# Performance work log

Hardware: AMD Instinct MI355X
Metric: run time of the kernel (lower is better)

The kernel has to match this reference:

```python
import jax, jax.numpy as jnp
import numpy as np

G, NPG, C, H, F, L = 256, 128, 16, 128, 128, 3
N = G * NPG          # 32768 nodes
E = 524288           # 16 edges per node on average
REG, REG_C = 0.01, 0.01
LN_EPS = 1e-5


def setup_inputs() -> dict:
    key = jax.random.key(0)
    ks = jax.random.split(key, 20)
    x = jax.random.normal(ks[0], (N, F), dtype=jnp.float32)
    # edges kept within each graph so dense pooling matches to_dense_batch semantics
    epg = E // G
    offs = jnp.repeat(jnp.arange(G, dtype=jnp.int64) * NPG, epg)
    src = jax.random.randint(ks[1], (E,), 0, NPG, dtype=jnp.int64) + offs
    tgt = jax.random.randint(ks[2], (E,), 0, NPG, dtype=jnp.int64) + offs
    edge_index = jnp.stack([src, tgt])
    mask_breaks = jax.random.bernoulli(ks[3], 0.5, (E,))
    s = jax.random.uniform(ks[4], (N, C), dtype=jnp.float32)
    batch = jnp.repeat(jnp.arange(G, dtype=jnp.int64), NPG)
    sc = 1.0 / np.sqrt(H)
    Wn = jax.random.normal(ks[5], (L, H, H), dtype=jnp.float32) * sc
    bn_ = jax.random.normal(ks[6], (L, H), dtype=jnp.float32) * sc
    Wo = jax.random.normal(ks[7], (L, H, H), dtype=jnp.float32) * sc
    bo = jax.random.normal(ks[8], (L, H), dtype=jnp.float32) * sc
    Wr = jax.random.normal(ks[9], (L, H, H), dtype=jnp.float32) * sc
    ln_g = jnp.ones((L, H), dtype=jnp.float32)
    ln_b = jnp.zeros((L, H), dtype=jnp.float32)
    fln_g = jnp.ones((H,), dtype=jnp.float32)
    fln_b = jnp.zeros((H,), dtype=jnp.float32)
    lin_w = jax.random.normal(ks[10], (1, H), dtype=jnp.float32) * sc
    bias = jnp.zeros((1,), dtype=jnp.float32)
    return {"x": x, "edge_index": edge_index, "mask_breaks": mask_breaks, "s": s,
            "batch": batch, "Wn": Wn, "bn_": bn_, "Wo": Wo, "bo": bo, "Wr": Wr,
            "ln_g": ln_g, "ln_b": ln_b, "fln_g": fln_g, "fln_b": fln_b,
            "lin_w": lin_w, "bias": bias}


def _layernorm(h, g, b):
    mu = jnp.mean(h, axis=-1, keepdims=True)
    v = jnp.mean(jnp.square(h - mu), axis=-1, keepdims=True)
    return (h - mu) * jax.lax.rsqrt(v + LN_EPS) * g + b


def reference(x, edge_index, mask_breaks, s, batch, Wn, bn_, Wo, bo, Wr,
              ln_g, ln_b, fln_g, fln_b, lin_w, bias):
    src, tgt = edge_index[0], edge_index[1]
    ones_e = jnp.ones((E,), dtype=x.dtype)
    cnt = jax.ops.segment_sum(ones_e, tgt, num_segments=N)          # in-degree
    inv_cnt = (1.0 / jnp.maximum(cnt, 1.0))[:, None]
    h = x
    for i in range(L):
        x_in = h @ Wn[i].T + bn_[i]
        x_out = h @ Wo[i].T + bo[i]
        x_root = h @ Wr[i].T
        msg = jnp.where(mask_breaks[:, None], x_in[src], x_out[src])  # [E,H]
        agg = jax.ops.segment_sum(msg, tgt, num_segments=N) * inv_cnt  # mean aggr
        h = jax.nn.relu(_layernorm(agg + x_root, ln_g[i], ln_b[i]))
    # dense per-graph views (equal-size graphs, batch ids sorted -> reshape)
    xd = h.reshape(G, NPG, H)
    sd = s.reshape(G, NPG, C)
    pooled = jnp.einsum("gnc,gnh->gch", sd, xd)                      # [G,C,H]
    pooled = _layernorm(pooled, fln_g, fln_b)
    xc = pooled @ lin_w.T                                            # [G,C,1]
    col_sum = sd.sum(axis=1)                                          # [G,C]
    cmask = (col_sum > 0)[..., None]
    xc = xc * cmask.astype(xc.dtype)
    out = xc.sum(axis=1) + bias                                      # [G,1]
    reg_loss = jnp.abs(Wo).sum() + jnp.abs(bo).sum()
    denom = (cmask.astype(xc.dtype).squeeze(-1) + 1e-7).sum(axis=1, keepdims=True)
    l1_loss = (jnp.abs(xc).sum(axis=1) / denom).mean()
    losses = REG * reg_loss + REG_C * l1_loss
    return out, losses, xc
```

## Files before the change

kernel.cpp:

```cpp
#include <hip/hip_runtime.h>

#define NN   32768
#define HD   128
#define EE   524288
#define GG   256
#define EPG  2048
#define CCd  16
#define LLd  3

typedef short short8 __attribute__((ext_vector_type(8)));
typedef float f32x4 __attribute__((ext_vector_type(4)));

__device__ __forceinline__ unsigned short f2bf(float f) {
  unsigned u = __builtin_bit_cast(unsigned, f);
  return (unsigned short)((u + 0x7FFFu + ((u >> 16) & 1u)) >> 16);
}
__device__ __forceinline__ unsigned bfpack(float a, float b) {
  return (unsigned)f2bf(a) | ((unsigned)f2bf(b) << 16);
}

__global__ __launch_bounds__(256) void convert_w_kernel(const float* __restrict__ Wn, const float* __restrict__ Wo,
                                                        const float* __restrict__ Wr, const float* __restrict__ bo,
                                                        unsigned* __restrict__ Wnb, unsigned* __restrict__ Wob,
                                                        unsigned* __restrict__ Wrb, float* __restrict__ wsreg) {
  int i = blockIdx.x * 256 + threadIdx.x;
  float4 a = *(const float4*)(Wn + (size_t)i * 4);
  float4 b = *(const float4*)(Wo + (size_t)i * 4);
  float4 c = *(const float4*)(Wr + (size_t)i * 4);
  *(uint2*)(Wnb + (size_t)i * 2) = make_uint2(bfpack(a.x, a.y), bfpack(a.z, a.w));
  *(uint2*)(Wob + (size_t)i * 2) = make_uint2(bfpack(b.x, b.y), bfpack(b.z, b.w));
  *(uint2*)(Wrb + (size_t)i * 2) = make_uint2(bfpack(c.x, c.y), bfpack(c.z, c.w));
  float s = fabsf(b.x) + fabsf(b.y) + fabsf(b.z) + fabsf(b.w);
  if (blockIdx.x == 0 && threadIdx.x < 96) {
    float4 d = *(const float4*)(bo + threadIdx.x * 4);
    s += fabsf(d.x) + fabsf(d.y) + fabsf(d.z) + fabsf(d.w);
  }
#pragma unroll
  for (int mk = 1; mk < 64; mk <<= 1) s += __shfl_xor(s, mk, 64);
  if ((threadIdx.x & 63) == 0) atomicAdd(wsreg, s);
}

__global__ __launch_bounds__(512, 2) void fused_kernel(
    const float* __restrict__ x,
    const int* __restrict__ esrc, const int* __restrict__ etgt, const int* __restrict__ emask,
    const unsigned short* __restrict__ Wnb, const unsigned short* __restrict__ Wob,
    const unsigned short* __restrict__ Wrb,
    const float* __restrict__ bn, const float* __restrict__ bo,
    const float* __restrict__ lng, const float* __restrict__ lnb,
    const float* __restrict__ s,
    const float* __restrict__ flng, const float* __restrict__ flnb,
    const float* __restrict__ linw, const float* __restrict__ bias,
    float* __restrict__ out, float* __restrict__ l1g) {
  __shared__ __align__(16) unsigned short hTs[128 * 136];
  __shared__ __align__(16) unsigned short sTs[16 * 136];
  __shared__ __align__(16) unsigned Mlds[2 * 128 * 64];
  __shared__ __align__(16) unsigned Wlds[128 * 64];
  __shared__ float finS[128], foutS[128];
  __shared__ float colsumS[CCd], xcs[CCd], axcs[CCd], msk[CCd];

  const int g = blockIdx.x;
  const int tid = threadIdx.x;
  const int wave = tid >> 6;
  const int lane = tid & 63;
  const int m = lane & 15;
  const int q = lane >> 4;
  const int t0 = wave << 4;

  const int wr = tid >> 2, wq = tid & 3, wsw = wr & 7;
  const int wbase = wr * 16 + wq * 4;
  uint4 wv0, wv1, wv2, wv3;
  {
    const uint4* wp = (const uint4*)Wnb;
    wv0 = wp[wbase + 0]; wv1 = wp[wbase + 1]; wv2 = wp[wbase + 2]; wv3 = wp[wbase + 3];
  }
  auto w_store = [&]() {
    *(uint4*)&Wlds[wr * 64 + (((wq * 4 + 0) ^ wsw) << 2)] = wv0;
    *(uint4*)&Wlds[wr * 64 + (((wq * 4 + 1) ^ wsw) << 2)] = wv1;
    *(uint4*)&Wlds[wr * 64 + (((wq * 4 + 2) ^ wsw) << 2)] = wv2;
    *(uint4*)&Wlds[wr * 64 + (((wq * 4 + 3) ^ wsw) << 2)] = wv3;
  };
  auto w_load = [&](const unsigned short* Wg) {
    const uint4* wp = (const uint4*)Wg;
    wv0 = wp[wbase + 0]; wv1 = wp[wbase + 1]; wv2 = wp[wbase + 2]; wv3 = wp[wbase + 3];
  };

  {
    uint4* cz = (uint4*)Mlds;
#pragma unroll
    for (int i = 0; i < 8; ++i) cz[i * 512 + tid] = make_uint4(0u, 0u, 0u, 0u);

    const float4* xg = (const float4*)(x + (size_t)g * 16384);
#pragma unroll
    for (int i = 0; i < 8; ++i) {
      int flat = i * 512 + tid;
      int t = flat >> 5, f0 = (flat & 31) << 2;
      float4 v = xg[flat];
      hTs[(f0 + 0) * 136 + t] = f2bf(v.x);
      hTs[(f0 + 1) * 136 + t] = f2bf(v.y);
      hTs[(f0 + 2) * 136 + t] = f2bf(v.z);
      hTs[(f0 + 3) * 136 + t] = f2bf(v.w);
    }
    {
      int t = tid >> 2, c0 = (tid & 3) << 2;
      float4 v = *(const float4*)(s + (size_t)g * 2048 + t * 16 + c0);
      sTs[(c0 + 0) * 136 + t] = f2bf(v.x);
      sTs[(c0 + 1) * 136 + t] = f2bf(v.y);
      sTs[(c0 + 2) * 136 + t] = f2bf(v.z);
      sTs[(c0 + 3) * 136 + t] = f2bf(v.w);
    }
    if (tid < 64) {
      int c = tid & 15, qq = tid >> 4;
      float cs = 0.f;
      for (int tt = qq; tt < 128; tt += 4) cs += s[(size_t)g * 2048 + tt * 16 + c];
      cs += __shfl_xor(cs, 16); cs += __shfl_xor(cs, 32);
      if (qq == 0) colsumS[c] = cs;
    }
  }
  __syncthreads();

  {
    const int e0 = g * EPG;
#pragma unroll
    for (int i = 0; i < 4; ++i) {
      int e = e0 + i * 512 + tid;
      int t = etgt[e] & 127;
      int sl = esrc[e] & 127;
      int dir = (emask[e] != 0) ? 0 : 1;
      atomicAdd(&Mlds[dir * 8192 + t * 64 + (((sl >> 3) ^ (t & 7)) << 2) + ((sl >> 1) & 3)],
                1u << ((sl & 1) * 16));
    }
  }
  __syncthreads();

  {
    const int t = t0 + m;
    const int base0 = t * 64 + q * 16;
    unsigned nin = 0, nout = 0;
#pragma unroll
    for (int k4 = 0; k4 < 4; ++k4) {
      uint4 a = *(const uint4*)&Mlds[base0 + k4 * 4];
      uint4 b = *(const uint4*)&Mlds[8192 + base0 + k4 * 4];
      nin  += (a.x & 0xffffu) + (a.x >> 16) + (a.y & 0xffffu) + (a.y >> 16)
            + (a.z & 0xffffu) + (a.z >> 16) + (a.w & 0xffffu) + (a.w >> 16);
      nout += (b.x & 0xffffu) + (b.x >> 16) + (b.y & 0xffffu) + (b.y >> 16)
            + (b.z & 0xffffu) + (b.z >> 16) + (b.w & 0xffffu) + (b.w >> 16);
    }
    nin  += __shfl_xor((int)nin, 16);  nin  += __shfl_xor((int)nin, 32);
    nout += __shfl_xor((int)nout, 16); nout += __shfl_xor((int)nout, 32);
    unsigned dg = nin + nout;
    float inv = 1.0f / (float)(dg > 0 ? dg : 1);
    if (q == 0) { finS[t] = (float)nin * inv; foutS[t] = (float)nout * inv; }
#pragma unroll
    for (int d = 0; d < 2; ++d)
#pragma unroll
      for (int k4 = 0; k4 < 4; ++k4) {
        unsigned* p = &Mlds[d * 8192 + base0 + k4 * 4];
        uint4 v = *(const uint4*)p;
        uint4 o;
        o.x = bfpack((float)(v.x & 0xffffu) * inv, (float)(v.x >> 16) * inv);
        o.y = bfpack((float)(v.y & 0xffffu) * inv, (float)(v.y >> 16) * inv);
        o.z = bfpack((float)(v.z & 0xffffu) * inv, (float)(v.z >> 16) * inv);
        o.w = bfpack((float)(v.w & 0xffffu) * inv, (float)(v.w >> 16) * inv);
        *(uint4*)p = o;
      }
  }
  __syncthreads();

  for (int L = 0; L < LLd; ++L) {
    f32x4 pre[8];
#pragma unroll
    for (int ct = 0; ct < 8; ++ct) pre[ct] = (f32x4){0.f, 0.f, 0.f, 0.f};
    f32x4 accT[8];

#pragma unroll
    for (int sg = 0; sg < 2; ++sg) {
#pragma unroll
      for (int ft = 0; ft < 8; ++ft) accT[ft] = (f32x4){0.f, 0.f, 0.f, 0.f};
#pragma unroll
      for (int hf = 0; hf < 2; ++hf)
#pragma unroll
        for (int ksl = 0; ksl < 2; ++ksl) {
          const int ksg = hf * 2 + ksl;
          short8 bfr = *(const short8*)&Mlds[sg * 8192 + (t0 + m) * 64 + (((ksg * 4 + q) ^ (m & 7)) << 2)];
#pragma unroll
          for (int ft = 0; ft < 8; ++ft) {
            short8 afr = *(const short8*)&hTs[(ft * 16 + m) * 136 + ksg * 32 + q * 8];
            accT[ft] = __builtin_amdgcn_mfma_f32_16x16x32_bf16(afr, bfr, accT[ft], 0, 0, 0);
          }
        }
      __syncthreads();
      w_store();
      w_load((sg == 0 ? Wob : Wrb) + L * 16384);
      __syncthreads();
#pragma unroll
      for (int hf = 0; hf < 2; ++hf)
#pragma unroll
        for (int ksl = 0; ksl < 2; ++ksl) {
          const int ksg = hf * 2 + ksl;
          f32x4 lo = accT[2 * ksg], hi = accT[2 * ksg + 1];
          short8 afr;
#pragma unroll
          for (int j = 0; j < 8; ++j) {
            int srcl = ((((q & 1) << 1) + (j >> 2)) << 4) + m;
            float ylo = __shfl(lo[j & 3], srcl, 64);
            float yhi = __shfl(hi[j & 3], srcl, 64);
            afr[j] = (short)f2bf((q >> 1) ? yhi : ylo);
          }
#pragma unroll
          for (int ct = 0; ct < 8; ++ct) {
            short8 bfr = *(const short8*)&Wlds[(ct * 16 + m) * 64 + (((ksg * 4 + q) ^ (m & 7)) << 2)];
            pre[ct] = __builtin_amdgcn_mfma_f32_16x16x32_bf16(afr, bfr, pre[ct], 0, 0, 0);
          }
        }
    }
    __syncthreads();
    w_store();
    if (L < LLd - 1) w_load(Wnb + (L + 1) * 16384);
    __syncthreads();
#pragma unroll
    for (int hf = 0; hf < 2; ++hf)
#pragma unroll
      for (int ksl = 0; ksl < 2; ++ksl) {
        const int ksg = hf * 2 + ksl;
        short8 afr;
#pragma unroll
        for (int j = 0; j < 8; ++j)
          afr[j] = (short)hTs[(ksg * 32 + q * 8 + j) * 136 + t0 + m];
#pragma unroll
        for (int ct = 0; ct < 8; ++ct) {
          short8 bfr = *(const short8*)&Wlds[(ct * 16 + m) * 64 + (((ksg * 4 + q) ^ (m & 7)) << 2)];
          pre[ct] = __builtin_amdgcn_mfma_f32_16x16x32_bf16(afr, bfr, pre[ct], 0, 0, 0);
        }
      }
    __syncthreads();
    {
      float bnv[8], bov[8], gv[8], bv[8];
#pragma unroll
      for (int ct = 0; ct < 8; ++ct) {
        int c = L * 128 + ct * 16 + m;
        bnv[ct] = bn[c]; bov[ct] = bo[c]; gv[ct] = lng[c]; bv[ct] = lnb[c];
      }
#pragma unroll
      for (int r = 0; r < 4; ++r) {
        const int tl = q * 4 + r;
        const float fiv = finS[t0 + tl], fov = foutS[t0 + tl];
        float v[8];
        float sum = 0.f;
#pragma unroll
        for (int ct = 0; ct < 8; ++ct) {
          v[ct] = pre[ct][r] + fiv * bnv[ct] + fov * bov[ct];
          sum += v[ct];
        }
        sum += __shfl_xor(sum, 1); sum += __shfl_xor(sum, 2);
        sum += __shfl_xor(sum, 4); sum += __shfl_xor(sum, 8);
        const float mu = sum * (1.0f / 128.0f);
        float sq = 0.f;
#pragma unroll
        for (int ct = 0; ct < 8; ++ct) { float d = v[ct] - mu; sq += d * d; }
        sq += __shfl_xor(sq, 1); sq += __shfl_xor(sq, 2);
        sq += __shfl_xor(sq, 4); sq += __shfl_xor(sq, 8);
        const float rstd = rsqrtf(sq * (1.0f / 128.0f) + 1e-5f);
#pragma unroll
        for (int ct = 0; ct < 8; ++ct) {
          float o = fmaxf((v[ct] - mu) * rstd * gv[ct] + bv[ct], 0.0f);
          hTs[(ct * 16 + m) * 136 + t0 + tl] = f2bf(o);
        }
      }
    }
    __syncthreads();
  }

  f32x4 pl = (f32x4){0.f, 0.f, 0.f, 0.f};
#pragma unroll
  for (int ks = 0; ks < 4; ++ks) {
    short8 a = *(const short8*)&sTs[m * 136 + ks * 32 + q * 8];
    short8 b = *(const short8*)&hTs[(wave * 16 + m) * 136 + ks * 32 + q * 8];
    pl = __builtin_amdgcn_mfma_f32_16x16x32_bf16(a, b, pl, 0, 0, 0);
  }
  float* pooledS = (float*)Mlds;
#pragma unroll
  for (int r = 0; r < 4; ++r) pooledS[(q * 4 + r) * 132 + wave * 16 + m] = pl[r];
  __syncthreads();

  if (tid < 256) {
    const int c = tid >> 4;
    const int j0 = (tid & 15) << 3;
    float v[8];
#pragma unroll
    for (int jj = 0; jj < 8; ++jj) v[jj] = pooledS[c * 132 + j0 + jj];
    float sum = 0.f;
#pragma unroll
    for (int jj = 0; jj < 8; ++jj) sum += v[jj];
#pragma unroll
    for (int mk = 1; mk < 16; mk <<= 1) sum += __shfl_xor(sum, mk, 64);
    float mu = sum * (1.0f / 128.0f);
    float sq = 0.f;
#pragma unroll
    for (int jj = 0; jj < 8; ++jj) { float d = v[jj] - mu; sq += d * d; }
#pragma unroll
    for (int mk = 1; mk < 16; mk <<= 1) sq += __shfl_xor(sq, mk, 64);
    float rstd = rsqrtf(sq * (1.0f / 128.0f) + 1e-5f);
    float dot = 0.f;
#pragma unroll
    for (int jj = 0; jj < 8; ++jj) {
      float nv = (v[jj] - mu) * rstd * flng[j0 + jj] + flnb[j0 + jj];
      dot += nv * linw[j0 + jj];
    }
#pragma unroll
    for (int mk = 1; mk < 16; mk <<= 1) dot += __shfl_xor(dot, mk, 64);
    if ((tid & 15) == 0) {
      float cm = (colsumS[c] > 0.f) ? 1.0f : 0.0f;
      float xcv = dot * cm;
      out[257 + g * CCd + c] = xcv;
      xcs[c] = xcv; axcs[c] = fabsf(xcv); msk[c] = cm;
    }
  }
  __syncthreads();
  if (tid == 0) {
    float so = 0.f, sa = 0.f, sd = 0.f;
#pragma unroll
    for (int k = 0; k < CCd; ++k) { so += xcs[k]; sa += axcs[k]; sd += msk[k] + 1e-7f; }
    out[g] = so + bias[0];
    l1g[g] = sa / sd;
  }
}

__global__ __launch_bounds__(256) void combine_kernel(const float* __restrict__ l1g, const float* __restrict__ wsreg,
                                                      float* __restrict__ outp) {
  const int tid = threadIdx.x;
  float s2 = l1g[tid];
#pragma unroll
  for (int mk = 1; mk < 64; mk <<= 1) s2 += __shfl_xor(s2, mk, 64);
  __shared__ float rs2[4];
  if ((tid & 63) == 0) rs2[tid >> 6] = s2;
  __syncthreads();
  if (tid == 0) {
    float l1 = (rs2[0] + rs2[1] + rs2[2] + rs2[3]) * (1.0f / GG);
    outp[0] = 0.01f * wsreg[0] + 0.01f * l1;
  }
}

extern "C" void kernel_launch(void* const* d_in, const int* in_sizes, int n_in,
                              void* d_out, int out_size, void* d_ws, size_t ws_size,
                              hipStream_t stream) {
  (void)in_sizes; (void)n_in; (void)out_size; (void)ws_size;
  const float* x    = (const float*)d_in[0];
  const int*   ei   = (const int*)d_in[1];
  const int*   mask = (const int*)d_in[2];
  const float* s    = (const float*)d_in[3];
  const float* Wn   = (const float*)d_in[5];
  const float* bn   = (const float*)d_in[6];
  const float* Wo   = (const float*)d_in[7];
  const float* bo   = (const float*)d_in[8];
  const float* Wr   = (const float*)d_in[9];
  const float* lng  = (const float*)d_in[10];
  const float* lnb  = (const float*)d_in[11];
  const float* flng = (const float*)d_in[12];
  const float* flnb = (const float*)d_in[13];
  const float* linw = (const float*)d_in[14];
  const float* bias = (const float*)d_in[15];
  float* out = (float*)d_out;

  char* ws = (char*)d_ws;
  size_t off = 0;
  auto alloc = [&](size_t b) { char* p = ws + off; off += (b + 255) & ~(size_t)255; return p; };
  unsigned short* Wnb = (unsigned short*)alloc((size_t)LLd * HD * HD * 2);
  unsigned short* Wob = (unsigned short*)alloc((size_t)LLd * HD * HD * 2);
  unsigned short* Wrb = (unsigned short*)alloc((size_t)LLd * HD * HD * 2);
  float* l1g    = (float*)alloc((size_t)GG * 4);
  float* wsreg  = (float*)alloc(256);

  const int* srcA = ei;
  const int* tgtA = ei + EE;

  hipMemsetAsync(wsreg, 0, 4, stream);
  convert_w_kernel<<<LLd * HD * HD / (256 * 4), 256, 0, stream>>>(Wn, Wo, Wr, bo,
      (unsigned*)Wnb, (unsigned*)Wob, (unsigned*)Wrb, wsreg);
  fused_kernel<<<GG, 512, 0, stream>>>(x, srcA, tgtA, mask, Wnb, Wob, Wrb, bn, bo,
                                       lng, lnb, s, flng, flnb, linw, bias, out, l1g);
  combine_kernel<<<1, 256, 0, stream>>>(l1g, wsreg, out + 256);
}
```

Before: 146.0 us.

## Fold weight conversion and loss combine into single fused kernel; swizzle hT layout

Removes the separate weight-conversion and combine kernels: each block now loads fp32 weights directly and converts them to bf16 when staging into LDS, computes a slice of the L1 regularizer, and the last block to finish (via an atomic ticket) writes the final loss. The transposed activation buffer switches from padded rows to an XOR-swizzled 128-wide layout, and the degree-count reads now use the same swizzle that was used when the counts were written. This cuts two launches and a global round trip, but doubles the per-block weight read bytes and adds conversion work inside the main loop.

```diff
diff --git a/kernel.cpp b/kernel.cpp
--- a/kernel.cpp
+++ b/kernel.cpp
@@ -19,39 +19,24 @@
   return (unsigned)f2bf(a) | ((unsigned)f2bf(b) << 16);
 }
 
-__global__ __launch_bounds__(256) void convert_w_kernel(const float* __restrict__ Wn, const float* __restrict__ Wo,
-                                                        const float* __restrict__ Wr, const float* __restrict__ bo,
-                                                        unsigned* __restrict__ Wnb, unsigned* __restrict__ Wob,
-                                                        unsigned* __restrict__ Wrb, float* __restrict__ wsreg) {
-  int i = blockIdx.x * 256 + threadIdx.x;
-  float4 a = *(const float4*)(Wn + (size_t)i * 4);
-  float4 b = *(const float4*)(Wo + (size_t)i * 4);
-  float4 c = *(const float4*)(Wr + (size_t)i * 4);
-  *(uint2*)(Wnb + (size_t)i * 2) = make_uint2(bfpack(a.x, a.y), bfpack(a.z, a.w));
-  *(uint2*)(Wob + (size_t)i * 2) = make_uint2(bfpack(b.x, b.y), bfpack(b.z, b.w));
-  *(uint2*)(Wrb + (size_t)i * 2) = make_uint2(bfpack(c.x, c.y), bfpack(c.z, c.w));
-  float s = fabsf(b.x) + fabsf(b.y) + fabsf(b.z) + fabsf(b.w);
-  if (blockIdx.x == 0 && threadIdx.x < 96) {
-    float4 d = *(const float4*)(bo + threadIdx.x * 4);
-    s += fabsf(d.x) + fabsf(d.y) + fabsf(d.z) + fabsf(d.w);
-  }
-#pragma unroll
-  for (int mk = 1; mk < 64; mk <<= 1) s += __shfl_xor(s, mk, 64);
-  if ((threadIdx.x & 63) == 0) atomicAdd(wsreg, s);
-}
-
-__global__ __launch_bounds__(512, 2) void fused_kernel(
+__device__ __forceinline__ int hchunk(int f, int c) {
+  return f * 128 + (((c & 8) | ((c ^ f ^ (f >> 3)) & 7)) << 3);
+}
+__device__ __forceinline__ int hidx(int f, int t) {
+  return hchunk(f, t >> 3) + (t & 7);
+}
+
+__global__ __launch_bounds__(512) void fused_kernel(
     const float* __restrict__ x,
     const int* __restrict__ esrc, const int* __restrict__ etgt, const int* __restrict__ emask,
-    const unsigned short* __restrict__ Wnb, const unsigned short* __restrict__ Wob,
-    const unsigned short* __restrict__ Wrb,
+    const float* __restrict__ Wn, const float* __restrict__ Wo, const float* __restrict__ Wr,
     const float* __restrict__ bn, const float* __restrict__ bo,
     const float* __restrict__ lng, const float* __restrict__ lnb,
     const float* __restrict__ s,
     const float* __restrict__ flng, const float* __restrict__ flnb,
     const float* __restrict__ linw, const float* __restrict__ bias,
-    float* __restrict__ out, float* __restrict__ l1g) {
-  __shared__ __align__(16) unsigned short hTs[128 * 136];
+    float* __restrict__ out, float* __restrict__ acc ) {
+  __shared__ __align__(16) unsigned short hTs[128 * 128];
   __shared__ __align__(16) unsigned short sTs[16 * 136];
   __shared__ __align__(16) unsigned Mlds[2 * 128 * 64];
   __shared__ __align__(16) unsigned Wlds[128 * 64];
@@ -67,22 +52,41 @@
   const int t0 = wave << 4;
 
   const int wr = tid >> 2, wq = tid & 3, wsw = wr & 7;
-  const int wbase = wr * 16 + wq * 4;
-  uint4 wv0, wv1, wv2, wv3;
+  float4 wf[8];
+  auto w_load = [&](const float* Wg) {
+    const float4* wp = (const float4*)(Wg + wr * 128 + wq * 32);
+#pragma unroll
+    for (int u = 0; u < 8; ++u) wf[u] = wp[u];
+  };
+  auto w_store = [&]() {
+#pragma unroll
+    for (int c = 0; c < 4; ++c) {
+      uint4 o;
+      o.x = bfpack(wf[c * 2].x, wf[c * 2].y);
+      o.y = bfpack(wf[c * 2].z, wf[c * 2].w);
+      o.z = bfpack(wf[c * 2 + 1].x, wf[c * 2 + 1].y);
+      o.w = bfpack(wf[c * 2 + 1].z, wf[c * 2 + 1].w);
+      *(uint4*)&Wlds[wr * 64 + (((wq * 4 + c) ^ wsw) << 2)] = o;
+    }
+  };
+  w_load(Wn);
+
   {
-    const uint4* wp = (const uint4*)Wnb;
-    wv0 = wp[wbase + 0]; wv1 = wp[wbase + 1]; wv2 = wp[wbase + 2]; wv3 = wp[wbase + 3];
-  }
-  auto w_store = [&]() {
-    *(uint4*)&Wlds[wr * 64 + (((wq * 4 + 0) ^ wsw) << 2)] = wv0;
-    *(uint4*)&Wlds[wr * 64 + (((wq * 4 + 1) ^ wsw) << 2)] = wv1;
-    *(uint4*)&Wlds[wr * 64 + (((wq * 4 + 2) ^ wsw) << 2)] = wv2;
-    *(uint4*)&Wlds[wr * 64 + (((wq * 4 + 3) ^ wsw) << 2)] = wv3;
-  };
-  auto w_load = [&](const unsigned short* Wg) {
-    const uint4* wp = (const uint4*)Wg;
-    wv0 = wp[wbase + 0]; wv1 = wp[wbase + 1]; wv2 = wp[wbase + 2]; wv3 = wp[wbase + 3];
-  };
+    float rsum = 0.f;
+    if (tid < 48) {
+      float4 v = ((const float4*)Wo)[g * 48 + tid];
+      rsum = fabsf(v.x) + fabsf(v.y) + fabsf(v.z) + fabsf(v.w);
+    }
+    if (g < 96 && tid == 48) {
+      float4 d = *(const float4*)(bo + g * 4);
+      rsum = fabsf(d.x) + fabsf(d.y) + fabsf(d.z) + fabsf(d.w);
+    }
+    if (tid < 64) {
+#pragma unroll
+      for (int mk = 1; mk < 64; mk <<= 1) rsum += __shfl_xor(rsum, mk, 64);
+      if (tid == 0) atomicAdd(&acc[0], rsum);
+    }
+  }
 
   {
     uint4* cz = (uint4*)Mlds;
@@ -95,10 +99,10 @@
       int flat = i * 512 + tid;
       int t = flat >> 5, f0 = (flat & 31) << 2;
       float4 v = xg[flat];
-      hTs[(f0 + 0) * 136 + t] = f2bf(v.x);
-      hTs[(f0 + 1) * 136 + t] = f2bf(v.y);
-      hTs[(f0 + 2) * 136 + t] = f2bf(v.z);
-      hTs[(f0 + 3) * 136 + t] = f2bf(v.w);
+      hTs[hidx(f0 + 0, t)] = f2bf(v.x);
+      hTs[hidx(f0 + 1, t)] = f2bf(v.y);
+      hTs[hidx(f0 + 2, t)] = f2bf(v.z);
+      hTs[hidx(f0 + 3, t)] = f2bf(v.w);
     }
     {
       int t = tid >> 2, c0 = (tid & 3) << 2;
@@ -134,12 +138,13 @@
 
   {
     const int t = t0 + m;
-    const int base0 = t * 64 + q * 16;
+    const int mm = m & 7;
     unsigned nin = 0, nout = 0;
 #pragma unroll
     for (int k4 = 0; k4 < 4; ++k4) {
-      uint4 a = *(const uint4*)&Mlds[base0 + k4 * 4];
-      uint4 b = *(const uint4*)&Mlds[8192 + base0 + k4 * 4];
+      int sl = (((q * 4 + k4) ^ mm) & 15) << 2;
+      uint4 a = *(const uint4*)&Mlds[t * 64 + sl];
+      uint4 b = *(const uint4*)&Mlds[8192 + t * 64 + sl];
       nin  += (a.x & 0xffffu) + (a.x >> 16) + (a.y & 0xffffu) + (a.y >> 16)
             + (a.z & 0xffffu) + (a.z >> 16) + (a.w & 0xffffu) + (a.w >> 16);
       nout += (b.x & 0xffffu) + (b.x >> 16) + (b.y & 0xffffu) + (b.y >> 16)
@@ -154,7 +159,8 @@
     for (int d = 0; d < 2; ++d)
 #pragma unroll
       for (int k4 = 0; k4 < 4; ++k4) {
-        unsigned* p = &Mlds[d * 8192 + base0 + k4 * 4];
+        int sl = (((q * 4 + k4) ^ mm) & 15) << 2;
+        unsigned* p = &Mlds[d * 8192 + t * 64 + sl];
         uint4 v = *(const uint4*)p;
         uint4 o;
         o.x = bfpack((float)(v.x & 0xffffu) * inv, (float)(v.x >> 16) * inv);
@@ -184,13 +190,13 @@
           short8 bfr = *(const short8*)&Mlds[sg * 8192 + (t0 + m) * 64 + (((ksg * 4 + q) ^ (m & 7)) << 2)];
 #pragma unroll
           for (int ft = 0; ft < 8; ++ft) {
-            short8 afr = *(const short8*)&hTs[(ft * 16 + m) * 136 + ksg * 32 + q * 8];
+            short8 afr = *(const short8*)&hTs[hchunk(ft * 16 + m, ksg * 4 + q)];
             accT[ft] = __builtin_amdgcn_mfma_f32_16x16x32_bf16(afr, bfr, accT[ft], 0, 0, 0);
           }
         }
       __syncthreads();
       w_store();
-      w_load((sg == 0 ? Wob : Wrb) + L * 16384);
+      w_load((sg == 0 ? Wo : Wr) + L * 16384);
       __syncthreads();
 #pragma unroll
       for (int hf = 0; hf < 2; ++hf)
@@ -215,7 +221,7 @@
     }
     __syncthreads();
     w_store();
-    if (L < LLd - 1) w_load(Wnb + (L + 1) * 16384);
+    if (L < LLd - 1) w_load(Wn + (L + 1) * 16384);
     __syncthreads();
 #pragma unroll
     for (int hf = 0; hf < 2; ++hf)
@@ -225,7 +231,7 @@
         short8 afr;
 #pragma unroll
         for (int j = 0; j < 8; ++j)
-          afr[j] = (short)hTs[(ksg * 32 + q * 8 + j) * 136 + t0 + m];
+          afr[j] = (short)hTs[hidx(ksg * 32 + q * 8 + j, t0 + m)];
 #pragma unroll
         for (int ct = 0; ct < 8; ++ct) {
           short8 bfr = *(const short8*)&Wlds[(ct * 16 + m) * 64 + (((ksg * 4 + q) ^ (m & 7)) << 2)];
@@ -263,7 +269,7 @@
 #pragma unroll
         for (int ct = 0; ct < 8; ++ct) {
           float o = fmaxf((v[ct] - mu) * rstd * gv[ct] + bv[ct], 0.0f);
-          hTs[(ct * 16 + m) * 136 + t0 + tl] = f2bf(o);
+          hTs[hidx(ct * 16 + m, t0 + tl)] = f2bf(o);
         }
       }
     }
@@ -274,7 +280,7 @@
 #pragma unroll
   for (int ks = 0; ks < 4; ++ks) {
     short8 a = *(const short8*)&sTs[m * 136 + ks * 32 + q * 8];
-    short8 b = *(const short8*)&hTs[(wave * 16 + m) * 136 + ks * 32 + q * 8];
+    short8 b = *(const short8*)&hTs[hchunk(wave * 16 + m, ks * 4 + q)];
     pl = __builtin_amdgcn_mfma_f32_16x16x32_bf16(a, b, pl, 0, 0, 0);
   }
   float* pooledS = (float*)Mlds;
@@ -316,27 +322,20 @@
     }
   }
   __syncthreads();
+
   if (tid == 0) {
     float so = 0.f, sa = 0.f, sd = 0.f;
 #pragma unroll
     for (int k = 0; k < CCd; ++k) { so += xcs[k]; sa += axcs[k]; sd += msk[k] + 1e-7f; }
     out[g] = so + bias[0];
-    l1g[g] = sa / sd;
-  }
-}
-
-__global__ __launch_bounds__(256) void combine_kernel(const float* __restrict__ l1g, const float* __restrict__ wsreg,
-                                                      float* __restrict__ outp) {
-  const int tid = threadIdx.x;
-  float s2 = l1g[tid];
-#pragma unroll
-  for (int mk = 1; mk < 64; mk <<= 1) s2 += __shfl_xor(s2, mk, 64);
-  __shared__ float rs2[4];
-  if ((tid & 63) == 0) rs2[tid >> 6] = s2;
-  __syncthreads();
-  if (tid == 0) {
-    float l1 = (rs2[0] + rs2[1] + rs2[2] + rs2[3]) * (1.0f / GG);
-    outp[0] = 0.01f * wsreg[0] + 0.01f * l1;
+    atomicAdd(&acc[1], sa / sd);
+    __threadfence();
+    unsigned tk = atomicAdd((unsigned*)&acc[2], 1u);
+    if (tk == GG - 1) {
+      float rg = atomicAdd(&acc[0], 0.0f);
+      float l1 = atomicAdd(&acc[1], 0.0f);
+      out[256] = 0.01f * rg + 0.01f * (l1 * (1.0f / GG));
+    }
   }
 }
 
@@ -361,22 +360,12 @@
   const float* bias = (const float*)d_in[15];
   float* out = (float*)d_out;
 
-  char* ws = (char*)d_ws;
-  size_t off = 0;
-  auto alloc = [&](size_t b) { char* p = ws + off; off += (b + 255) & ~(size_t)255; return p; };
-  unsigned short* Wnb = (unsigned short*)alloc((size_t)LLd * HD * HD * 2);
-  unsigned short* Wob = (unsigned short*)alloc((size_t)LLd * HD * HD * 2);
-  unsigned short* Wrb = (unsigned short*)alloc((size_t)LLd * HD * HD * 2);
-  float* l1g    = (float*)alloc((size_t)GG * 4);
-  float* wsreg  = (float*)alloc(256);
+  float* acc = (float*)d_ws;
 
   const int* srcA = ei;
   const int* tgtA = ei + EE;
 
-  hipMemsetAsync(wsreg, 0, 4, stream);
-  convert_w_kernel<<<LLd * HD * HD / (256 * 4), 256, 0, stream>>>(Wn, Wo, Wr, bo,
-      (unsigned*)Wnb, (unsigned*)Wob, (unsigned*)Wrb, wsreg);
-  fused_kernel<<<GG, 512, 0, stream>>>(x, srcA, tgtA, mask, Wnb, Wob, Wrb, bn, bo,
-                                       lng, lnb, s, flng, flnb, linw, bias, out, l1g);
-  combine_kernel<<<1, 256, 0, stream>>>(l1g, wsreg, out + 256);
-}
+  hipMemsetAsync(acc, 0, 16, stream);
+  fused_kernel<<<GG, 512, 0, stream>>>(x, srcA, tgtA, mask, Wn, Wo, Wr, bn, bo,
+                                       lng, lnb, s, flng, flnb, linw, bias, out, acc);
+}
```

After: 159.3 us. +9.2%, slower.

## Read weight fragments directly from global memory and swizzle the hidden-state LDS tile

Applied to the files above, without the earlier changes.

Removes the LDS weight staging buffer and its per-stage register-prefetch/store with the surrounding barriers, so MFMA B fragments are loaded straight from global (L2-resident) bf16 weights. The hidden-state tile moves from a padded 136-stride layout to an XOR-swizzled 128-stride layout, and the transposed accumulator is packed to bf16 before the cross-lane shuffle, halving the shuffle count. Dropping the second launch bound and the weight buffer frees LDS and barriers, but puts global-load latency on the MFMA inner loop and leaves the register budget to the compiler.

```diff
diff --git a/kernel.cpp b/kernel.cpp
--- a/kernel.cpp
+++ b/kernel.cpp
@@ -17,6 +17,13 @@
 }
 __device__ __forceinline__ unsigned bfpack(float a, float b) {
   return (unsigned)f2bf(a) | ((unsigned)f2bf(b) << 16);
+}
+
+__device__ __forceinline__ int hchunk(int f, int c) {
+  return f * 128 + (((c & 8) | ((c ^ f ^ (f >> 3)) & 7)) << 3);
+}
+__device__ __forceinline__ int hidx(int f, int t) {
+  return hchunk(f, t >> 3) + (t & 7);
 }
 
 __global__ __launch_bounds__(256) void convert_w_kernel(const float* __restrict__ Wn, const float* __restrict__ Wo,
@@ -40,7 +47,7 @@
   if ((threadIdx.x & 63) == 0) atomicAdd(wsreg, s);
 }
 
-__global__ __launch_bounds__(512, 2) void fused_kernel(
+__global__ __launch_bounds__(512) void fused_kernel(
     const float* __restrict__ x,
     const int* __restrict__ esrc, const int* __restrict__ etgt, const int* __restrict__ emask,
     const unsigned short* __restrict__ Wnb, const unsigned short* __restrict__ Wob,
@@ -51,10 +58,9 @@
     const float* __restrict__ flng, const float* __restrict__ flnb,
     const float* __restrict__ linw, const float* __restrict__ bias,
     float* __restrict__ out, float* __restrict__ l1g) {
-  __shared__ __align__(16) unsigned short hTs[128 * 136];
+  __shared__ __align__(16) unsigned short hTs[128 * 128];
   __shared__ __align__(16) unsigned short sTs[16 * 136];
   __shared__ __align__(16) unsigned Mlds[2 * 128 * 64];
-  __shared__ __align__(16) unsigned Wlds[128 * 64];
   __shared__ float finS[128], foutS[128];
   __shared__ float colsumS[CCd], xcs[CCd], axcs[CCd], msk[CCd];
 
@@ -66,24 +72,6 @@
   const int q = lane >> 4;
   const int t0 = wave << 4;
 
-  const int wr = tid >> 2, wq = tid & 3, wsw = wr & 7;
-  const int wbase = wr * 16 + wq * 4;
-  uint4 wv0, wv1, wv2, wv3;
-  {
-    const uint4* wp = (const uint4*)Wnb;
-    wv0 = wp[wbase + 0]; wv1 = wp[wbase + 1]; wv2 = wp[wbase + 2]; wv3 = wp[wbase + 3];
-  }
-  auto w_store = [&]() {
-    *(uint4*)&Wlds[wr * 64 + (((wq * 4 + 0) ^ wsw) << 2)] = wv0;
-    *(uint4*)&Wlds[wr * 64 + (((wq * 4 + 1) ^ wsw) << 2)] = wv1;
-    *(uint4*)&Wlds[wr * 64 + (((wq * 4 + 2) ^ wsw) << 2)] = wv2;
-    *(uint4*)&Wlds[wr * 64 + (((wq * 4 + 3) ^ wsw) << 2)] = wv3;
-  };
-  auto w_load = [&](const unsigned short* Wg) {
-    const uint4* wp = (const uint4*)Wg;
-    wv0 = wp[wbase + 0]; wv1 = wp[wbase + 1]; wv2 = wp[wbase + 2]; wv3 = wp[wbase + 3];
-  };
-
   {
     uint4* cz = (uint4*)Mlds;
 #pragma unroll
@@ -95,10 +83,10 @@
       int flat = i * 512 + tid;
       int t = flat >> 5, f0 = (flat & 31) << 2;
       float4 v = xg[flat];
-      hTs[(f0 + 0) * 136 + t] = f2bf(v.x);
-      hTs[(f0 + 1) * 136 + t] = f2bf(v.y);
-      hTs[(f0 + 2) * 136 + t] = f2bf(v.z);
-      hTs[(f0 + 3) * 136 + t] = f2bf(v.w);
+      hTs[hidx(f0 + 0, t)] = f2bf(v.x);
+      hTs[hidx(f0 + 1, t)] = f2bf(v.y);
+      hTs[hidx(f0 + 2, t)] = f2bf(v.z);
+      hTs[hidx(f0 + 3, t)] = f2bf(v.w);
     }
     {
       int t = tid >> 2, c0 = (tid & 3) << 2;
@@ -134,12 +122,13 @@
 
   {
     const int t = t0 + m;
-    const int base0 = t * 64 + q * 16;
+    const int mm = m & 7;
     unsigned nin = 0, nout = 0;
 #pragma unroll
     for (int k4 = 0; k4 < 4; ++k4) {
-      uint4 a = *(const uint4*)&Mlds[base0 + k4 * 4];
-      uint4 b = *(const uint4*)&Mlds[8192 + base0 + k4 * 4];
+      int sl = (((q * 4 + k4) ^ mm) & 15) << 2;
+      uint4 a = *(const uint4*)&Mlds[t * 64 + sl];
+      uint4 b = *(const uint4*)&Mlds[8192 + t * 64 + sl];
       nin  += (a.x & 0xffffu) + (a.x >> 16) + (a.y & 0xffffu) + (a.y >> 16)
             + (a.z & 0xffffu) + (a.z >> 16) + (a.w & 0xffffu) + (a.w >> 16);
       nout += (b.x & 0xffffu) + (b.x >> 16) + (b.y & 0xffffu) + (b.y >> 16)
@@ -154,7 +143,8 @@
     for (int d = 0; d < 2; ++d)
 #pragma unroll
       for (int k4 = 0; k4 < 4; ++k4) {
-        unsigned* p = &Mlds[d * 8192 + base0 + k4 * 4];
+        int sl = (((q * 4 + k4) ^ mm) & 15) << 2;
+        unsigned* p = &Mlds[d * 8192 + t * 64 + sl];
         uint4 v = *(const uint4*)p;
         uint4 o;
         o.x = bfpack((float)(v.x & 0xffffu) * inv, (float)(v.x >> 16) * inv);
@@ -174,6 +164,7 @@
 
 #pragma unroll
     for (int sg = 0; sg < 2; ++sg) {
+      const unsigned short* Wg = (sg == 0 ? Wnb : Wob) + L * 16384;
 #pragma unroll
       for (int ft = 0; ft < 8; ++ft) accT[ft] = (f32x4){0.f, 0.f, 0.f, 0.f};
 #pragma unroll
@@ -184,54 +175,51 @@
           short8 bfr = *(const short8*)&Mlds[sg * 8192 + (t0 + m) * 64 + (((ksg * 4 + q) ^ (m & 7)) << 2)];
 #pragma unroll
           for (int ft = 0; ft < 8; ++ft) {
-            short8 afr = *(const short8*)&hTs[(ft * 16 + m) * 136 + ksg * 32 + q * 8];
+            short8 afr = *(const short8*)&hTs[hchunk(ft * 16 + m, ksg * 4 + q)];
             accT[ft] = __builtin_amdgcn_mfma_f32_16x16x32_bf16(afr, bfr, accT[ft], 0, 0, 0);
           }
         }
-      __syncthreads();
-      w_store();
-      w_load((sg == 0 ? Wob : Wrb) + L * 16384);
-      __syncthreads();
 #pragma unroll
       for (int hf = 0; hf < 2; ++hf)
 #pragma unroll
         for (int ksl = 0; ksl < 2; ++ksl) {
           const int ksg = hf * 2 + ksl;
           f32x4 lo = accT[2 * ksg], hi = accT[2 * ksg + 1];
+          unsigned pk[4];
+#pragma unroll
+          for (int r = 0; r < 4; ++r) pk[r] = bfpack(lo[r], hi[r]);
           short8 afr;
 #pragma unroll
           for (int j = 0; j < 8; ++j) {
             int srcl = ((((q & 1) << 1) + (j >> 2)) << 4) + m;
-            float ylo = __shfl(lo[j & 3], srcl, 64);
-            float yhi = __shfl(hi[j & 3], srcl, 64);
-            afr[j] = (short)f2bf((q >> 1) ? yhi : ylo);
+            unsigned v = (unsigned)__shfl((int)pk[j & 3], srcl, 64);
+            afr[j] = (short)(unsigned short)((q >> 1) ? (v >> 16) : (v & 0xffffu));
           }
 #pragma unroll
           for (int ct = 0; ct < 8; ++ct) {
-            short8 bfr = *(const short8*)&Wlds[(ct * 16 + m) * 64 + (((ksg * 4 + q) ^ (m & 7)) << 2)];
+            short8 bfr = *(const short8*)&Wg[(ct * 16 + m) * 128 + ksg * 32 + q * 8];
             pre[ct] = __builtin_amdgcn_mfma_f32_16x16x32_bf16(afr, bfr, pre[ct], 0, 0, 0);
           }
         }
     }
-    __syncthreads();
-    w_store();
-    if (L < LLd - 1) w_load(Wnb + (L + 1) * 16384);
-    __syncthreads();
-#pragma unroll
-    for (int hf = 0; hf < 2; ++hf)
-#pragma unroll
-      for (int ksl = 0; ksl < 2; ++ksl) {
-        const int ksg = hf * 2 + ksl;
-        short8 afr;
-#pragma unroll
-        for (int j = 0; j < 8; ++j)
-          afr[j] = (short)hTs[(ksg * 32 + q * 8 + j) * 136 + t0 + m];
-#pragma unroll
-        for (int ct = 0; ct < 8; ++ct) {
-          short8 bfr = *(const short8*)&Wlds[(ct * 16 + m) * 64 + (((ksg * 4 + q) ^ (m & 7)) << 2)];
-          pre[ct] = __builtin_amdgcn_mfma_f32_16x16x32_bf16(afr, bfr, pre[ct], 0, 0, 0);
-        }
-      }
+    {
+      const unsigned short* Wrg = Wrb + L * 16384;
+#pragma unroll
+      for (int hf = 0; hf < 2; ++hf)
+#pragma unroll
+        for (int ksl = 0; ksl < 2; ++ksl) {
+          const int ksg = hf * 2 + ksl;
+          short8 afr;
+#pragma unroll
+          for (int j = 0; j < 8; ++j)
+            afr[j] = (short)hTs[hidx(ksg * 32 + q * 8 + j, t0 + m)];
+#pragma unroll
+          for (int ct = 0; ct < 8; ++ct) {
+            short8 bfr = *(const short8*)&Wrg[(ct * 16 + m) * 128 + ksg * 32 + q * 8];
+            pre[ct] = __builtin_amdgcn_mfma_f32_16x16x32_bf16(afr, bfr, pre[ct], 0, 0, 0);
+          }
+        }
+    }
     __syncthreads();
     {
       float bnv[8], bov[8], gv[8], bv[8];
@@ -263,7 +251,7 @@
 #pragma unroll
         for (int ct = 0; ct < 8; ++ct) {
           float o = fmaxf((v[ct] - mu) * rstd * gv[ct] + bv[ct], 0.0f);
-          hTs[(ct * 16 + m) * 136 + t0 + tl] = f2bf(o);
+          hTs[hidx(ct * 16 + m, t0 + tl)] = f2bf(o);
         }
       }
     }
@@ -274,7 +262,7 @@
 #pragma unroll
   for (int ks = 0; ks < 4; ++ks) {
     short8 a = *(const short8*)&sTs[m * 136 + ks * 32 + q * 8];
-    short8 b = *(const short8*)&hTs[(wave * 16 + m) * 136 + ks * 32 + q * 8];
+    short8 b = *(const short8*)&hTs[hchunk(wave * 16 + m, ks * 4 + q)];
     pl = __builtin_amdgcn_mfma_f32_16x16x32_bf16(a, b, pl, 0, 0, 0);
   }
   float* pooledS = (float*)Mlds;
```

Measured after the change: 265.5 us. 81.9% more time.
